# Kernel optimization log

Measured on AMD Instinct MI355X. Metric: run time of the kernel, lower is better.

The kernel has to match this reference:

```python
import jax, jax.numpy as jnp
import numpy as np

EMBED_DIM = 1024
NUM_HEADS = 16
HEAD_DIM = EMBED_DIM // NUM_HEADS
BATCH = 2
SEQ = 2048


def setup_inputs() -> dict:
    key = jax.random.key(0)
    ks = jax.random.split(key, 10)
    s = 1.0 / np.sqrt(EMBED_DIM)
    inp = {
        "query": jax.random.normal(ks[0], (BATCH, SEQ, EMBED_DIM), jnp.float32),
        # Linear weights stored as [in, out] (y = x @ W + b)
        "wq": jax.random.normal(ks[1], (EMBED_DIM, EMBED_DIM), jnp.float32) * s,
        "bq": jnp.zeros((EMBED_DIM,), jnp.float32),
        "wk": jax.random.normal(ks[2], (EMBED_DIM, EMBED_DIM), jnp.float32) * s,
        "bk": jnp.zeros((EMBED_DIM,), jnp.float32),
        "wv": jax.random.normal(ks[3], (EMBED_DIM, EMBED_DIM), jnp.float32) * s,
        "bv": jnp.zeros((EMBED_DIM,), jnp.float32),
        "wo": jax.random.normal(ks[4], (EMBED_DIM, EMBED_DIM), jnp.float32) * s,
        "bo": jnp.zeros((EMBED_DIM,), jnp.float32),
        "temperature": jnp.float32(HEAD_DIM),  # learnable temperature, init = head_dim
    }
    return inp


def reference(query, wq, bq, wk, bk, wv, bv, wo, bo, temperature):
    B, S, E = query.shape
    # self-attention: key = value = query
    Q = (query @ wq + bq).reshape(B, S, NUM_HEADS, HEAD_DIM).transpose(0, 2, 1, 3)
    K = (query @ wk + bk).reshape(B, S, NUM_HEADS, HEAD_DIM).transpose(0, 2, 1, 3)
    V = (query @ wv + bv).reshape(B, S, NUM_HEADS, HEAD_DIM).transpose(0, 2, 1, 3)
    # squared Euclidean distances: ||q||^2 + ||k||^2 - 2<q,k>
    q_sq = jnp.sum(Q * Q, axis=-1, keepdims=True)          # (B,H,Sq,1)
    k_sq = jnp.sum(K * K, axis=-1, keepdims=True)          # (B,H,Sk,1)
    qk = jnp.einsum("bhqd,bhkd->bhqk", Q, K)
    d_sq = jnp.maximum(q_sq + jnp.swapaxes(k_sq, -2, -1) - 2.0 * qk, 0.0)
    attn = jax.nn.softmax(-d_sq / temperature, axis=-1)    # (B,H,Sq,Sk)
    out = jnp.einsum("bhqk,bhkd->bhqd", attn, V)
    out = out.transpose(0, 2, 1, 3).reshape(B, S, E)
    return out @ wo + bo
```

## Files before the change

kernel.cpp:

```cpp
#include <hip/hip_runtime.h>
#include <stdint.h>
#include <stddef.h>


#define LOG2E 1.44269504088896f

typedef __attribute__((ext_vector_type(8))) short bf16x8;
typedef __attribute__((ext_vector_type(4))) float f32x4;
typedef __attribute__((ext_vector_type(4))) unsigned short u16x4;

__device__ __forceinline__ unsigned short f2b(float f) {
  union { float f; unsigned int u; } x; x.f = f;
  unsigned int u = x.u;
  u += 0x7fffu + ((u >> 16) & 1u);
  return (unsigned short)(u >> 16);
}
__device__ __forceinline__ float b2f(unsigned short s) {
  union { unsigned int u; float f; } x; x.u = ((unsigned int)s) << 16;
  return x.f;
}
__device__ __forceinline__ unsigned int fbits(float f) {
  union { float f; unsigned int u; } x; x.f = f; return x.u;
}

#define GLD_LDS(g, l) __builtin_amdgcn_global_load_lds( \
    (const __attribute__((address_space(1))) void*)(g), \
    (__attribute__((address_space(3))) void*)(l), 16, 0, 0)

__global__ void prep_kernel(const float* __restrict__ X,
                            const float* __restrict__ wq, const float* __restrict__ wk,
                            const float* __restrict__ wv, const float* __restrict__ wo,
                            unsigned short* __restrict__ Xb,
                            unsigned short* __restrict__ WTqkv, unsigned short* __restrict__ WTo) {
  int z = blockIdx.z;
  if (z == 4) {
    size_t base = ((size_t)(blockIdx.y * 16 + blockIdx.x)) * 16384;
    #pragma unroll
    for (int j = 0; j < 16; ++j) {
      size_t i = base + (size_t)(j * 256 + threadIdx.x) * 4;
      f32x4 v = *(const f32x4*)&X[i];
      u16x4 o;
      #pragma unroll
      for (int k = 0; k < 4; ++k) o[k] = f2b(v[k]);
      *(u16x4*)&Xb[i] = o;
    }
    return;
  }
  __shared__ float tile[64][65];
  const float* src = (z == 0) ? wq : (z == 1) ? wk : (z == 2) ? wv : wo;
  unsigned short* dst = (z < 3) ? (WTqkv + (size_t)z * 1024 * 1024) : WTo;
  int k0 = blockIdx.y * 64, n0 = blockIdx.x * 64;
  int tr = threadIdx.x >> 4;
  int tc4 = (threadIdx.x & 15) * 4;
  #pragma unroll
  for (int p = 0; p < 4; ++p) {
    int row = p * 16 + tr;
    f32x4 v = *(const f32x4*)&src[(size_t)(k0 + row) * 1024 + n0 + tc4];
    #pragma unroll
    for (int j = 0; j < 4; ++j) tile[row][tc4 + j] = v[j];
  }
  __syncthreads();
  #pragma unroll
  for (int p = 0; p < 4; ++p) {
    int nr = p * 16 + tr;
    u16x4 o;
    #pragma unroll
    for (int j = 0; j < 4; ++j) o[j] = f2b(tile[tc4 + j][nr]);
    *(u16x4*)&dst[(size_t)(n0 + nr) * 1024 + k0 + tc4] = o;
  }
}

__global__ __launch_bounds__(256, 3) void gemm_qkv_kernel(
    const unsigned short* __restrict__ X, const unsigned short* __restrict__ WT,
    const float* __restrict__ bq, const float* __restrict__ bk, const float* __restrict__ bv,
    const float* __restrict__ temp,
    unsigned short* __restrict__ Qb, unsigned short* __restrict__ Kb,
    unsigned short* __restrict__ VTo, float* __restrict__ ks2) {
  __shared__ __align__(16) unsigned short smem3[24576];
#define AS3(j) (smem3 + (j) * 4096)
#define BS3(j) (smem3 + 12288 + (j) * 4096)
  const int t = threadIdx.x, w = t >> 6, lane = t & 63;
  const int r = lane & 15, q4 = lane >> 4;
  const int m0 = blockIdx.y * 128, n0 = blockIdx.x * 128;
  const int wr = (w >> 1) * 64, wc = (w & 1) * 64;
  const unsigned short* Xg = X + (size_t)m0 * 1024;
  const unsigned short* Wg = WT + (size_t)n0 * 1024;
  const int swz = ((t & 3) ^ ((t >> 2) & 3)) * 8;
  const unsigned short* xs0 = Xg + (size_t)(t >> 2) * 1024 + swz;
  const unsigned short* xs1 = xs0 + (size_t)64 * 1024;
  const unsigned short* ws0 = Wg + (size_t)(t >> 2) * 1024 + swz;
  const unsigned short* ws1 = ws0 + (size_t)64 * 1024;
  f32x4 acc[4][4] = {};

#define QKV_STAGE(J2)                                     \
  {                                                       \
    GLD_LDS(xs0, &AS3(J2)[(w * 64) * 8]);                 \
    GLD_LDS(xs1, &AS3(J2)[(256 + w * 64) * 8]);           \
    GLD_LDS(ws0, &BS3(J2)[(w * 64) * 8]);                 \
    GLD_LDS(ws1, &BS3(J2)[(256 + w * 64) * 8]);           \
    xs0 += 32; xs1 += 32; ws0 += 32; ws1 += 32;           \
  }

  QKV_STAGE(0)
  QKV_STAGE(1)
  asm volatile("s_waitcnt vmcnt(4)" ::: "memory");
  __builtin_amdgcn_s_barrier();
  __builtin_amdgcn_sched_barrier(0);

  const int ru = (q4 ^ (r & 3)) * 8;

#define QKV_BODY(J, STG, LAST)                                                \
  {                                                                           \
    if (STG) QKV_STAGE(((J) + 2) % 3)                                         \
    bf16x8 af[4], bfr[4];                                                     \
    _Pragma("unroll")                                                         \
    for (int mf = 0; mf < 4; ++mf)                                            \
      af[mf] = *(const bf16x8*)&AS3(J)[(wr + mf * 16 + r) * 32 + ru];         \
    _Pragma("unroll")                                                         \
    for (int nf = 0; nf < 4; ++nf)                                            \
      bfr[nf] = *(const bf16x8*)&BS3(J)[(wc + nf * 16 + r) * 32 + ru];        \
    _Pragma("unroll")                                                         \
    for (int mf = 0; mf < 4; ++mf)                                            \
      _Pragma("unroll")                                                       \
      for (int nf = 0; nf < 4; ++nf)                                          \
        acc[mf][nf] = __builtin_amdgcn_mfma_f32_16x16x32_bf16(af[mf], bfr[nf], acc[mf][nf], 0, 0, 0); \
    if (STG)       { asm volatile("s_waitcnt vmcnt(4)" ::: "memory"); }       \
    else if (!(LAST)) { asm volatile("s_waitcnt vmcnt(0)" ::: "memory"); }    \
    if (!(LAST)) {                                                            \
      __builtin_amdgcn_s_barrier();                                           \
      __builtin_amdgcn_sched_barrier(0);                                      \
    }                                                                         \
  }

  for (int hh = 0; hh < 5; ++hh) {
    QKV_BODY(0, 1, 0) QKV_BODY(1, 1, 0) QKV_BODY(2, 1, 0)
    QKV_BODY(0, 1, 0) QKV_BODY(1, 1, 0) QKV_BODY(2, 1, 0)
  }
  QKV_BODY(0, 0, 0)
  QKV_BODY(1, 0, 1)
  __syncthreads();
#undef QKV_BODY
#undef QKV_STAGE

  const int nblk = n0 >> 10;
  if (nblk == 0) {
    const int nc0 = n0 & 1023;
    #pragma unroll
    for (int nf = 0; nf < 4; ++nf) {
      int n = nc0 + wc + nf * 16 + r;
      float bb = bq[n];
      #pragma unroll
      for (int mf = 0; mf < 4; ++mf) {
        int m = m0 + wr + mf * 16 + q4 * 4;
        f32x4 v = acc[mf][nf];
        #pragma unroll
        for (int i = 0; i < 4; ++i)
          Qb[(size_t)(m + i) * 1024 + n] = f2b(v[i] + bb);
      }
    }
  } else if (nblk == 1) {
    const float sc = LOG2E / temp[0];
    const int nc0 = n0 & 1023;
    float s2a[4][4] = {};
    #pragma unroll
    for (int nf = 0; nf < 4; ++nf) {
      int n = nc0 + wc + nf * 16 + r;
      float bb = bk[n];
      #pragma unroll
      for (int mf = 0; mf < 4; ++mf) {
        int m = m0 + wr + mf * 16 + q4 * 4;
        f32x4 v = acc[mf][nf];
        #pragma unroll
        for (int i = 0; i < 4; ++i) {
          unsigned short os = f2b(v[i] + bb);
          Kb[(size_t)(m + i) * 1024 + n] = os;
          float xb = b2f(os);
          s2a[mf][i] += xb * xb;
        }
      }
    }
    #pragma unroll
    for (int mf = 0; mf < 4; ++mf)
      #pragma unroll
      for (int i = 0; i < 4; ++i) {
        float v = s2a[mf][i];
        v += __shfl_xor(v, 1, 64);
        v += __shfl_xor(v, 2, 64);
        v += __shfl_xor(v, 4, 64);
        v += __shfl_xor(v, 8, 64);
        s2a[mf][i] = v * sc;
      }
    if (r == 0) {
      int hh2 = (nc0 + wc) >> 6;
      #pragma unroll
      for (int mf = 0; mf < 4; ++mf) {
        int m = m0 + wr + mf * 16 + q4 * 4;
        int bb2 = m >> 11, ss = m & 2047;
        #pragma unroll
        for (int i = 0; i < 4; ++i)
          ks2[(size_t)(bb2 * 16 + hh2) * 2048 + ss + i] = s2a[mf][i];
      }
    }
  } else {
    unsigned short* Vt = smem3;
    const int c0 = n0 - 2048;
    const int head = w & 1;
    #pragma unroll
    for (int nf = 0; nf < 4; ++nf) {
      int c = c0 + wc + nf * 16 + r;
      float bb = bv[c];
      int d = c & 63;
      #pragma unroll
      for (int mf = 0; mf < 4; ++mf) {
        int mloc = wr + mf * 16 + q4 * 4;
        int G = mloc >> 6;
        int k6 = mloc & 63;
        int pos = (k6 >> 5) * 32 + ((k6 & 15) >> 2) * 8 + ((k6 >> 4) & 1) * 4;
        f32x4 v = acc[mf][nf];
        u16x4 pk;
        #pragma unroll
        for (int i = 0; i < 4; ++i) pk[i] = f2b(v[i] + bb);
        *(u16x4*)&Vt[(head * 64 + d) * 132 + G * 64 + pos] = pk;
      }
    }
    __syncthreads();
    int row = t >> 1, ch = t & 1;
    int hd = row >> 6, dd = row & 63;
    int hglob = (c0 >> 6) + hd;
    int bb2 = m0 >> 11, s0 = m0 & 2047;
    unsigned short* dst = &VTo[((size_t)((bb2 * 16 + hglob) * 64 + dd)) * 2048 + s0 + ch * 64];
    const unsigned short* srcL = &Vt[(hd * 64 + dd) * 132 + ch * 64];
    #pragma unroll
    for (int k2 = 0; k2 < 16; ++k2)
      *(u16x4*)&dst[k2 * 4] = *(const u16x4*)&srcL[k2 * 4];
  }
#undef AS3
#undef BS3
}

__global__ __launch_bounds__(256, 2) void flash_kernel(
    const unsigned short* __restrict__ Qb, const unsigned short* __restrict__ Kb,
    const unsigned short* __restrict__ VT, const float* __restrict__ ks2,
    const float* __restrict__ temp, unsigned short* __restrict__ AO) {
  __shared__ __align__(16) unsigned short Ks[3][64 * 64];
  __shared__ __align__(16) unsigned short Vs[3][64 * 64];
  __shared__ __align__(16) float KQs[2048];
  const int t = threadIdx.x, w = t >> 6, lane = t & 63;
  const int r = lane & 15, q4 = lane >> 4;
  const int wgid = blockIdx.x + 16 * blockIdx.y;
  const int xcd = wgid & 7, s = wgid >> 3;
  const int bh = xcd + 8 * (s & 3);
  const int b = bh >> 4, h = bh & 15;
  const int q0 = (s >> 2) * 128;
  const float cc = 2.0f * LOG2E / temp[0];

  bf16x8 qf[2][2];
  #pragma unroll
  for (int qg = 0; qg < 2; ++qg) {
    int sq = q0 + w * 32 + qg * 16 + r;
    const unsigned short* qp = Qb + (size_t)(b * 2048 + sq) * 1024 + h * 64;
    #pragma unroll
    for (int ks = 0; ks < 2; ++ks) qf[qg][ks] = *(const bf16x8*)(qp + ks * 32 + q4 * 8);
  }

  f32x4 accO[2][4] = {};
  f32x4 lsum[2] = {};
  bf16x8 ones;
  #pragma unroll
  for (int j = 0; j < 8; ++j) ones[j] = (short)0x3F80;

  const unsigned short* Kg = Kb + ((size_t)b * 2048) * 1024 + h * 64;
  const unsigned short* Vg = VT + ((size_t)bh * 64) * 2048;
  const float* kqb = ks2 + bh * 2048;

  const unsigned short* kp0 = Kg + (size_t)(t >> 2) * 1024 + (t & 3) * 8;
  const unsigned short* kp1 = kp0 + 32;
  int dd0 = t >> 3;
  const unsigned short* vp0 = Vg + (size_t)dd0 * 2048 + ((t & 7) ^ (dd0 & 7)) * 8;
  const unsigned short* vp1 = vp0 + (size_t)32 * 2048;

  GLD_LDS(kqb + t * 4, &KQs[t * 4]);
  GLD_LDS(kqb + 1024 + t * 4, &KQs[1024 + t * 4]);
  GLD_LDS(kp0, &Ks[0][t * 8]);
  GLD_LDS(kp1, &Ks[0][(256 + t) * 8]);
  GLD_LDS(vp0, &Vs[0][t * 8]);
  GLD_LDS(vp1, &Vs[0][(256 + t) * 8]);
  kp0 += 65536; kp1 += 65536; vp0 += 64; vp1 += 64;
  GLD_LDS(kp0, &Ks[1][t * 8]);
  GLD_LDS(kp1, &Ks[1][(256 + t) * 8]);
  GLD_LDS(vp0, &Vs[1][t * 8]);
  GLD_LDS(vp1, &Vs[1][(256 + t) * 8]);
  kp0 += 65536; kp1 += 65536; vp0 += 64; vp1 += 64;
  asm volatile("s_waitcnt vmcnt(4)" ::: "memory");
  __builtin_amdgcn_s_barrier();
  __builtin_amdgcn_sched_barrier(0);

#define CHUNK_BODY(C, J, STG, LAST)                                           \
  {                                                                           \
    const int c_ = (C);                                                       \
    if (STG) {                                                                \
      GLD_LDS(kp0, &Ks[((J) + 2) % 3][t * 8]);                                \
      GLD_LDS(kp1, &Ks[((J) + 2) % 3][(256 + t) * 8]);                        \
      GLD_LDS(vp0, &Vs[((J) + 2) % 3][t * 8]);                                \
      GLD_LDS(vp1, &Vs[((J) + 2) % 3][(256 + t) * 8]);                        \
      kp0 += 65536; kp1 += 65536; vp0 += 64; vp1 += 64;                       \
    }                                                                         \
          \
    f32x4 st[2][4];                                                           \
    {                                                                         \
      const f32x4 zz = {};                                                    \
      __builtin_amdgcn_s_setprio(1);                                          \
      _Pragma("unroll")                                                       \
      for (int ks = 0; ks < 2; ++ks) {                                        \
        _Pragma("unroll")                                                     \
        for (int kfm = 0; kfm < 4; ++kfm) {                                   \
          bf16x8 ka = *(const bf16x8*)&Ks[(J)][(ks * 64 + kfm * 16 + r) * 32 + q4 * 8]; \
          st[0][kfm] = __builtin_amdgcn_mfma_f32_16x16x32_bf16(ka, qf[0][ks], ks ? st[0][kfm] : zz, 0, 0, 0); \
          st[1][kfm] = __builtin_amdgcn_mfma_f32_16x16x32_bf16(ka, qf[1][ks], ks ? st[1][kfm] : zz, 0, 0, 0); \
        }                                                                     \
      }                                                                       \
      __builtin_amdgcn_s_setprio(0);                                          \
    }                                                                         \
                 \
    f32x4 kq[4];                                                              \
    _Pragma("unroll")                                                         \
    for (int kfm = 0; kfm < 4; ++kfm)                                         \
      kq[kfm] = *(const f32x4*)&KQs[c_ * 64 + kfm * 16 + q4 * 4];             \
    bf16x8 pf[2][2];                                                          \
    _Pragma("unroll")                                                         \
    for (int qg = 0; qg < 2; ++qg) {                                          \
      _Pragma("unroll")                                                       \
      for (int cb = 0; cb < 2; ++cb) {                                        \
        unsigned int dw[4];                                                   \
        _Pragma("unroll")                                                     \
        for (int half = 0; half < 2; ++half) {                                \
          int kfm = cb * 2 + half;                                            \
          float pp[4];                                                        \
          _Pragma("unroll")                                                   \
          for (int i = 0; i < 4; ++i) {                                       \
            float u = __builtin_fmaf(cc, st[qg][kfm][i], -kq[kfm][i]);        \
            pp[i] = __builtin_amdgcn_exp2f(u);                                \
          }                                                                   \
          dw[half * 2 + 0] = (fbits(pp[0]) >> 16) | (fbits(pp[1]) & 0xFFFF0000u); \
          dw[half * 2 + 1] = (fbits(pp[2]) >> 16) | (fbits(pp[3]) & 0xFFFF0000u); \
        }                                                                     \
        union { unsigned int d[4]; bf16x8 v; } cv;                            \
        cv.d[0] = dw[0]; cv.d[1] = dw[1]; cv.d[2] = dw[2]; cv.d[3] = dw[3];   \
        pf[qg][cb] = cv.v;                                                    \
      }                                                                       \
    }                                                                         \
                                        \
    __builtin_amdgcn_s_setprio(1);                                            \
    _Pragma("unroll")                                                         \
    for (int cb = 0; cb < 2; ++cb) {                                          \
      lsum[0] = __builtin_amdgcn_mfma_f32_16x16x32_bf16(pf[0][cb], ones, lsum[0], 0, 0, 0); \
      lsum[1] = __builtin_amdgcn_mfma_f32_16x16x32_bf16(pf[1][cb], ones, lsum[1], 0, 0, 0); \
      _Pragma("unroll")                                                       \
      for (int df = 0; df < 4; ++df) {                                        \
        int dloc = df * 16 + r;                                               \
        int un = dloc * 8 + ((cb * 4 + q4) ^ (dloc & 7));                     \
        bf16x8 vb = *(const bf16x8*)&Vs[(J)][un * 8];                         \
        accO[0][df] = __builtin_amdgcn_mfma_f32_16x16x32_bf16(pf[0][cb], vb, accO[0][df], 0, 0, 0); \
        accO[1][df] = __builtin_amdgcn_mfma_f32_16x16x32_bf16(pf[1][cb], vb, accO[1][df], 0, 0, 0); \
      }                                                                       \
    }                                                                         \
    __builtin_amdgcn_s_setprio(0);                                            \
                             \
    if (STG)          { asm volatile("s_waitcnt vmcnt(4)" ::: "memory"); }    \
    else if (!(LAST)) { asm volatile("s_waitcnt vmcnt(0)" ::: "memory"); }    \
    if (!(LAST)) {                                                            \
      __builtin_amdgcn_s_barrier();                                           \
      __builtin_amdgcn_sched_barrier(0);                                      \
    }                                                                         \
  }

  for (int c3 = 0; c3 < 10; ++c3) {
    CHUNK_BODY(3 * c3 + 0, 0, 1, 0)
    CHUNK_BODY(3 * c3 + 1, 1, 1, 0)
    CHUNK_BODY(3 * c3 + 2, 2, 1, 0)
  }
  CHUNK_BODY(30, 0, 0, 0)
  CHUNK_BODY(31, 1, 0, 1)
#undef CHUNK_BODY

  {
    #pragma unroll
    for (int qg = 0; qg < 2; ++qg) {
      float inv[4];
      #pragma unroll
      for (int i = 0; i < 4; ++i) inv[i] = 1.0f / lsum[qg][i];
      #pragma unroll
      for (int df = 0; df < 4; ++df) {
        int d = df * 16 + r;
        #pragma unroll
        for (int i = 0; i < 4; ++i) {
          int sq = q0 + w * 32 + qg * 16 + q4 * 4 + i;
          AO[(size_t)(b * 2048 + sq) * 1024 + h * 64 + d] = f2b(accO[qg][df][i] * inv[i]);
        }
      }
    }
  }
}

__global__ __launch_bounds__(256, 2) void gemm_out_kernel(
    const unsigned short* __restrict__ A, const unsigned short* __restrict__ WT,
    const float* __restrict__ bo, float* __restrict__ Out) {
  __shared__ __align__(16) unsigned short osmem[18432];
#define AS3o(j) (osmem + (j) * 4096)
#define BS3o(j) (osmem + 12288 + (j) * 2048)
  const int t = threadIdx.x, w = t >> 6, lane = t & 63;
  const int r = lane & 15, q4 = lane >> 4;
  const int m0 = blockIdx.y * 128, n0 = blockIdx.x * 64;
  const int wr = (w >> 1) * 64, wc = (w & 1) * 32;
  const unsigned short* Ag = A + (size_t)m0 * 1024;
  const unsigned short* Wg = WT + (size_t)n0 * 1024;
  const int swz = ((t & 3) ^ ((t >> 2) & 3)) * 8;
  const unsigned short* as0 = Ag + (size_t)(t >> 2) * 1024 + swz;
  const unsigned short* as1 = as0 + (size_t)64 * 1024;
  const unsigned short* bs0 = Wg + (size_t)(t >> 2) * 1024 + swz;
  f32x4 acc[4][2] = {};

#define OUT_STAGE(J2)                                     \
  {                                                       \
    GLD_LDS(as0, &AS3o(J2)[(w * 64) * 8]);                \
    GLD_LDS(as1, &AS3o(J2)[(256 + w * 64) * 8]);          \
    GLD_LDS(bs0, &BS3o(J2)[(w * 64) * 8]);                \
    as0 += 32; as1 += 32; bs0 += 32;                      \
  }

  OUT_STAGE(0)
  OUT_STAGE(1)
  asm volatile("s_waitcnt vmcnt(3)" ::: "memory");
  __builtin_amdgcn_s_barrier();
  __builtin_amdgcn_sched_barrier(0);

  const int ru = (q4 ^ (r & 3)) * 8;

#define OUT_BODY(J, STG, LAST)                                                \
  {                                                                           \
    if (STG) OUT_STAGE(((J) + 2) % 3)                                         \
    bf16x8 af[4], bfr[2];                                                     \
    _Pragma("unroll")                                                         \
    for (int mf = 0; mf < 4; ++mf)                                            \
      af[mf] = *(const bf16x8*)&AS3o(J)[(wr + mf * 16 + r) * 32 + ru];        \
    _Pragma("unroll")                                                         \
    for (int nf = 0; nf < 2; ++nf)                                            \
      bfr[nf] = *(const bf16x8*)&BS3o(J)[(wc + nf * 16 + r) * 32 + ru];       \
    _Pragma("unroll")                                                         \
    for (int mf = 0; mf < 4; ++mf)                                            \
      _Pragma("unroll")                                                       \
      for (int nf = 0; nf < 2; ++nf)                                          \
        acc[mf][nf] = __builtin_amdgcn_mfma_f32_16x16x32_bf16(af[mf], bfr[nf], acc[mf][nf], 0, 0, 0); \
    if (STG)       { asm volatile("s_waitcnt vmcnt(3)" ::: "memory"); }       \
    else if (!(LAST)) { asm volatile("s_waitcnt vmcnt(0)" ::: "memory"); }    \
    if (!(LAST)) {                                                            \
      __builtin_amdgcn_s_barrier();                                           \
      __builtin_amdgcn_sched_barrier(0);                                      \
    }                                                                         \
  }

  for (int hh = 0; hh < 5; ++hh) {
    OUT_BODY(0, 1, 0) OUT_BODY(1, 1, 0) OUT_BODY(2, 1, 0)
    OUT_BODY(0, 1, 0) OUT_BODY(1, 1, 0) OUT_BODY(2, 1, 0)
  }
  OUT_BODY(0, 0, 0)
  OUT_BODY(1, 0, 1)
#undef OUT_BODY
#undef OUT_STAGE
#undef AS3o
#undef BS3o

  #pragma unroll
  for (int nf = 0; nf < 2; ++nf) {
    int n = n0 + wc + nf * 16 + r;
    float bb = bo[n];
    #pragma unroll
    for (int mf = 0; mf < 4; ++mf) {
      int m = m0 + wr + mf * 16 + q4 * 4;
      f32x4 v = acc[mf][nf];
      #pragma unroll
      for (int i = 0; i < 4; ++i)
        Out[(size_t)(m + i) * 1024 + n] = v[i] + bb;
    }
  }
}

extern "C" void kernel_launch(void* const* d_in, const int* in_sizes, int n_in,
                              void* d_out, int out_size, void* d_ws, size_t ws_size,
                              hipStream_t stream) {
  const float* X    = (const float*)d_in[0];
  const float* wq   = (const float*)d_in[1];
  const float* bq   = (const float*)d_in[2];
  const float* wk   = (const float*)d_in[3];
  const float* bk   = (const float*)d_in[4];
  const float* wv   = (const float*)d_in[5];
  const float* bv   = (const float*)d_in[6];
  const float* wo   = (const float*)d_in[7];
  const float* bo   = (const float*)d_in[8];
  const float* temp = (const float*)d_in[9];
  float* Out = (float*)d_out;

  char* ws = (char*)d_ws;
  unsigned short* Xb    = (unsigned short*)ws; ws += (size_t)4096 * 1024 * 2;
  unsigned short* WTqkv = (unsigned short*)ws; ws += (size_t)3072 * 1024 * 2;
  unsigned short* WTo   = (unsigned short*)ws; ws += (size_t)1024 * 1024 * 2;
  unsigned short* Qb    = (unsigned short*)ws; ws += (size_t)4096 * 1024 * 2;
  unsigned short* Kb    = (unsigned short*)ws; ws += (size_t)4096 * 1024 * 2;
  unsigned short* VT    = (unsigned short*)ws; ws += (size_t)4096 * 1024 * 2;
  float* ks2 = (float*)ws; ws += (size_t)65536 * 4;
  unsigned short* AO = Xb;

  prep_kernel<<<dim3(16, 16, 5), 256, 0, stream>>>(X, wq, wk, wv, wo, Xb, WTqkv, WTo);
  gemm_qkv_kernel<<<dim3(24, 32), 256, 0, stream>>>(Xb, WTqkv, bq, bk, bv, temp, Qb, Kb, VT, ks2);
  flash_kernel<<<dim3(16, 32), 256, 0, stream>>>(Qb, Kb, VT, ks2, temp, AO);
  gemm_out_kernel<<<dim3(16, 32), 256, 0, stream>>>(AO, WTo, bo, Out);
}
```

Before: 186.0 us.

## Shrink flash attention blocks to two waves and switch to double-buffered K/V

The flash kernel now runs 128-thread blocks covering 64 query rows each, twice as many blocks, with the workgroup-to-head mapping and grid adjusted to match. Staging of K/V tiles is rewritten for 128 threads, and the LDS ring drops from three buffers to two, with a full vmcnt(0) wait before each barrier. The aim is more resident blocks per CU and better load balance. The cost is that each K/V tile is fetched by twice as many blocks, and prefetch overlap is shallower because every chunk waits for the next load to finish.

```diff
diff --git a/kernel.cpp b/kernel.cpp
--- a/kernel.cpp
+++ b/kernel.cpp
@@ -238,20 +238,20 @@
 #undef BS3
 }
 
-__global__ __launch_bounds__(256, 2) void flash_kernel(
+__global__ __launch_bounds__(128, 2) void flash_kernel(
     const unsigned short* __restrict__ Qb, const unsigned short* __restrict__ Kb,
     const unsigned short* __restrict__ VT, const float* __restrict__ ks2,
     const float* __restrict__ temp, unsigned short* __restrict__ AO) {
-  __shared__ __align__(16) unsigned short Ks[3][64 * 64];
-  __shared__ __align__(16) unsigned short Vs[3][64 * 64];
+  __shared__ __align__(16) unsigned short Ks[2][64 * 64];
+  __shared__ __align__(16) unsigned short Vs[2][64 * 64];
   __shared__ __align__(16) float KQs[2048];
   const int t = threadIdx.x, w = t >> 6, lane = t & 63;
   const int r = lane & 15, q4 = lane >> 4;
-  const int wgid = blockIdx.x + 16 * blockIdx.y;
+  const int wgid = blockIdx.x + 32 * blockIdx.y;
   const int xcd = wgid & 7, s = wgid >> 3;
   const int bh = xcd + 8 * (s & 3);
   const int b = bh >> 4, h = bh & 15;
-  const int q0 = (s >> 2) * 128;
+  const int q0 = (s >> 2) * 64;
   const float cc = 2.0f * LOG2E / temp[0];
 
   bf16x8 qf[2][2];
@@ -277,34 +277,34 @@
   const unsigned short* kp1 = kp0 + 32;
   int dd0 = t >> 3;
   const unsigned short* vp0 = Vg + (size_t)dd0 * 2048 + ((t & 7) ^ (dd0 & 7)) * 8;
-  const unsigned short* vp1 = vp0 + (size_t)32 * 2048;
-
-  GLD_LDS(kqb + t * 4, &KQs[t * 4]);
+
+#define STAGE_CHUNK(BUF)                                                      \
+  {                                                                           \
+    GLD_LDS(kp0,                  &Ks[BUF][t * 8]);                           \
+    GLD_LDS(kp0 + 32 * 1024,      &Ks[BUF][(128 + t) * 8]);                   \
+    GLD_LDS(kp1,                  &Ks[BUF][(256 + t) * 8]);                   \
+    GLD_LDS(kp1 + 32 * 1024,      &Ks[BUF][(384 + t) * 8]);                   \
+    GLD_LDS(vp0,                  &Vs[BUF][t * 8]);                           \
+    GLD_LDS(vp0 + 16 * 2048,      &Vs[BUF][(128 + t) * 8]);                   \
+    GLD_LDS(vp0 + 32 * 2048,      &Vs[BUF][(256 + t) * 8]);                   \
+    GLD_LDS(vp0 + 48 * 2048,      &Vs[BUF][(384 + t) * 8]);                   \
+    kp0 += 65536; kp1 += 65536; vp0 += 64;                                    \
+  }
+
+  GLD_LDS(kqb + t * 4,        &KQs[t * 4]);
+  GLD_LDS(kqb + 512 + t * 4,  &KQs[512 + t * 4]);
   GLD_LDS(kqb + 1024 + t * 4, &KQs[1024 + t * 4]);
-  GLD_LDS(kp0, &Ks[0][t * 8]);
-  GLD_LDS(kp1, &Ks[0][(256 + t) * 8]);
-  GLD_LDS(vp0, &Vs[0][t * 8]);
-  GLD_LDS(vp1, &Vs[0][(256 + t) * 8]);
-  kp0 += 65536; kp1 += 65536; vp0 += 64; vp1 += 64;
-  GLD_LDS(kp0, &Ks[1][t * 8]);
-  GLD_LDS(kp1, &Ks[1][(256 + t) * 8]);
-  GLD_LDS(vp0, &Vs[1][t * 8]);
-  GLD_LDS(vp1, &Vs[1][(256 + t) * 8]);
-  kp0 += 65536; kp1 += 65536; vp0 += 64; vp1 += 64;
-  asm volatile("s_waitcnt vmcnt(4)" ::: "memory");
+  GLD_LDS(kqb + 1536 + t * 4, &KQs[1536 + t * 4]);
+  STAGE_CHUNK(0)
+  STAGE_CHUNK(1)
+  asm volatile("s_waitcnt vmcnt(8)" ::: "memory");
   __builtin_amdgcn_s_barrier();
   __builtin_amdgcn_sched_barrier(0);
 
 #define CHUNK_BODY(C, J, STG, LAST)                                           \
   {                                                                           \
     const int c_ = (C);                                                       \
-    if (STG) {                                                                \
-      GLD_LDS(kp0, &Ks[((J) + 2) % 3][t * 8]);                                \
-      GLD_LDS(kp1, &Ks[((J) + 2) % 3][(256 + t) * 8]);                        \
-      GLD_LDS(vp0, &Vs[((J) + 2) % 3][t * 8]);                                \
-      GLD_LDS(vp1, &Vs[((J) + 2) % 3][(256 + t) * 8]);                        \
-      kp0 += 65536; kp1 += 65536; vp0 += 64; vp1 += 64;                       \
-    }                                                                         \
+    if (STG) STAGE_CHUNK((J) ^ 1)                                             \
           \
     f32x4 st[2][4];                                                           \
     {                                                                         \
@@ -365,23 +365,22 @@
       }                                                                       \
     }                                                                         \
     __builtin_amdgcn_s_setprio(0);                                            \
-                             \
-    if (STG)          { asm volatile("s_waitcnt vmcnt(4)" ::: "memory"); }    \
-    else if (!(LAST)) { asm volatile("s_waitcnt vmcnt(0)" ::: "memory"); }    \
+                 \
     if (!(LAST)) {                                                            \
+      asm volatile("s_waitcnt vmcnt(0)" ::: "memory");                        \
       __builtin_amdgcn_s_barrier();                                           \
       __builtin_amdgcn_sched_barrier(0);                                      \
     }                                                                         \
   }
 
-  for (int c3 = 0; c3 < 10; ++c3) {
-    CHUNK_BODY(3 * c3 + 0, 0, 1, 0)
-    CHUNK_BODY(3 * c3 + 1, 1, 1, 0)
-    CHUNK_BODY(3 * c3 + 2, 2, 1, 0)
-  }
-  CHUNK_BODY(30, 0, 0, 0)
+  CHUNK_BODY(0, 0, 0, 0)
+  for (int c2 = 0; c2 < 15; ++c2) {
+    CHUNK_BODY(2 * c2 + 1, 1, 1, 0)
+    CHUNK_BODY(2 * c2 + 2, 0, 1, 0)
+  }
   CHUNK_BODY(31, 1, 0, 1)
 #undef CHUNK_BODY
+#undef STAGE_CHUNK
 
   {
     #pragma unroll
@@ -512,6 +511,6 @@
 
   prep_kernel<<<dim3(16, 16, 5), 256, 0, stream>>>(X, wq, wk, wv, wo, Xb, WTqkv, WTo);
   gemm_qkv_kernel<<<dim3(24, 32), 256, 0, stream>>>(Xb, WTqkv, bq, bk, bv, temp, Qb, Kb, VT, ks2);
-  flash_kernel<<<dim3(16, 32), 256, 0, stream>>>(Qb, Kb, VT, ks2, temp, AO);
+  flash_kernel<<<dim3(32, 32), 128, 0, stream>>>(Qb, Kb, VT, ks2, temp, AO);
   gemm_out_kernel<<<dim3(16, 32), 256, 0, stream>>>(AO, WTo, bo, Out);
 }
```

Result: no change. 187.0 us (+0.5%).
